# Optimization experiments

Hardware: AMD Instinct MI355X
Metric: run time of the kernel (lower is better)

The kernel has to match this reference:

```python
import jax, jax.numpy as jnp
import numpy as np

T, N, F = 16, 50000, 128
B, S0, S1 = 1024, 10, 5
H0, H1, C = 128, 64, 10
G, DELAYS, K = 8, (1, 3, 5), 5
TAU, ALPHA, VTH = 1.0, 1.0, 1.0


@jax.custom_vjp
def spike_fn(v):
    # Heaviside forward, triangle surrogate backward (alpha=1.0)
    return (v >= VTH).astype(v.dtype)

def _spk_fwd(v):
    return (v >= VTH).astype(v.dtype), v

def _spk_bwd(v, g):
    return (g * ALPHA * jnp.maximum(0.0, 1.0 - jnp.abs(v - VTH)),)

spike_fn.defvjp(_spk_fwd, _spk_bwd)


def setup_inputs() -> dict:
    key = jax.random.key(0)
    ks = jax.random.split(key, 12)
    sc = 0.1
    return {
        'x': jax.random.uniform(ks[0], (T, N, F), jnp.float32),
        'nodes': jax.random.randint(ks[1], (B,), 0, N, jnp.int32),
        'nbr1': jax.random.randint(ks[2], (T, B, S0), 0, N, jnp.int32),
        'nbr2': jax.random.randint(ks[3], (T, B * S0, S1), 0, N, jnp.int32),
        'W_self0': jax.random.normal(ks[4], (F, H0), jnp.float32) * sc,
        'W_neigh0': jax.random.normal(ks[5], (F, H0), jnp.float32) * sc,
        'b0': jnp.zeros((H0,), jnp.float32),
        'W_self1': jax.random.normal(ks[6], (H0, H1), jnp.float32) * sc,
        'W_neigh1': jax.random.normal(ks[7], (H0, H1), jnp.float32) * sc,
        'b1': jnp.zeros((H1,), jnp.float32),
        'delay_logits': jax.random.normal(ks[8], (G, len(DELAYS)), jnp.float32),
        'tsr_dw': jax.random.normal(ks[9], (H1, K), jnp.float32) * sc,
        'tsr_pw': jax.random.normal(ks[10], (H1, C), jnp.float32) * sc,
        'tsr_b': jnp.zeros((C,), jnp.float32),
    }


def reference(x, nodes, nbr1, nbr2, W_self0, W_neigh0, b0, W_self1, W_neigh1, b1,
              delay_logits, tsr_dw, tsr_pw, tsr_b):
    v0_init = jnp.zeros((B + B * S0, H0), x.dtype)
    v1_init = jnp.zeros((B, H1), x.dtype)

    def step(carry, inp):
        v0, v1 = carry
        xt, n1, n2 = inp
        # per-timestep neighbor gathers (irregular access)
        h0 = xt[nodes]                   # [B, F]
        h1 = xt[n1.reshape(-1)]          # [B*S0, F]
        h2 = xt[n2.reshape(-1)]          # [B*S0*S1, F]
        # layer 0: SAGE (mean aggr, concat=False) over both levels, then LIF
        self_x = jnp.concatenate([h0, h1], axis=0)
        neigh = jnp.concatenate([h1.reshape(B, S0, F).mean(1),
                                 h2.reshape(B * S0, S1, F).mean(1)], axis=0)
        a0 = self_x @ W_self0 + neigh @ W_neigh0 + b0
        v0c = v0 + (a0 - v0) / TAU
        spk0 = spike_fn(v0c)
        v0n = v0c * (1.0 - spk0)          # hard reset to 0
        # layer 1: SAGE over level-0 spikes, then LIF
        s_self, s_nb = spk0[:B], spk0[B:]
        a1 = s_self @ W_self1 + s_nb.reshape(B, S0, H0).mean(1) @ W_neigh1 + b1
        v1c = v1 + (a1 - v1) / TAU
        spk1 = spike_fn(v1c)
        v1n = v1c * (1.0 - spk1)
        return (v0n, v1n), spk1

    _, spikes = jax.lax.scan(step, (v0_init, v1_init), (x, nbr1, nbr2))
    spikes = jnp.transpose(spikes, (1, 0, 2))    # [B, T, H1]

    # GroupSparseDelay1D: per-group softmax mixture of time-shifted copies
    w = jax.nn.softmax(delay_logits, axis=-1)     # [G, n_delays]
    wch = jnp.repeat(w, H1 // G, axis=0)          # [H1, n_delays]
    delayed = jnp.zeros_like(spikes)
    for i, d in enumerate(DELAYS):
        shifted = jnp.pad(spikes, ((0, 0), (d, 0), (0, 0)))[:, :T, :]
        delayed = delayed + shifted * wch[:, i]
    spikes = delayed

    # TemporalSeparableReadout: depthwise temporal conv (k=5) + pointwise + mean over T
    xc = jnp.transpose(spikes, (0, 2, 1))         # [B, H1, T]
    y = jax.lax.conv_general_dilated(xc, tsr_dw[:, None, :], (1,), 'SAME',
                                     feature_group_count=H1)  # [B, H1, T]
    out = jnp.einsum('bdt,dc->bc', y, tsr_pw) / T + tsr_b      # [B, C]
    return out
```

## Files before the change

kernel.cpp:

```cpp
#include <hip/hip_runtime.h>
#include <math.h>

#define TT 16
#define NN 50000
#define FF 128
#define BB 1024
#define S0C 10
#define S1C 5
#define H0C 128
#define H1C 64
#define CCC 10
#define R0C (BB + BB*S0C)
#define BANDF 4e-3f

typedef __attribute__((ext_vector_type(8))) short bf16x8;
typedef __attribute__((ext_vector_type(4))) float f32x4;

__device__ __forceinline__ unsigned short bf16_rn(float f) {
  unsigned u = __float_as_uint(f);
  return (unsigned short)((u + 0x7FFFu + ((u >> 16) & 1u)) >> 16);
}
__device__ __forceinline__ void split2(float f, unsigned short& h, unsigned short& l) {
  h = bf16_rn(f);
  float hf = __uint_as_float((unsigned)h << 16);
  l = bf16_rn(f - hf);
}

__global__ __launch_bounds__(256) void k_prep_w(
    const float* __restrict__ Ws0, const float* __restrict__ Wn0,
    unsigned short* __restrict__ Wswz)
{
  const int id = blockIdx.x * 256 + threadIdx.x;
  if (id >= 256 * 128) return;
  const int k = id >> 7, n = id & 127;
  const float wv = (k < 128) ? Ws0[k * H0C + n] : Wn0[(k - 128) * H0C + n];
  unsigned short h, l;
  split2(wv, h, l);
  const int ks = k >> 5, kq = (k >> 3) & 3, j = k & 7;
  const int nt = n >> 4, n16 = n & 15;
  const int idx = (((ks * 8 + nt) * 64) + (kq * 16 + n16)) * 8 + j;
  Wswz[idx] = h;
  Wswz[32768 + idx] = l;
}

__global__ __launch_bounds__(256, 2) void k_layer0(
    const float* __restrict__ x, const int* __restrict__ nodes,
    const int* __restrict__ nbr1, const int* __restrict__ nbr2,
    const unsigned short* __restrict__ Wswz, const float* __restrict__ b0,
    unsigned char* __restrict__ spk0,
    unsigned int* __restrict__ band_list, unsigned int* __restrict__ band_cnt,
    int band_cap)
{
  __shared__ __align__(16) unsigned short Abf[2 * 64 * 256];
  const int t   = blockIdx.y;
  const int r0  = blockIdx.x * 64;
  const int tid = threadIdx.x;
  const float* xt = x + (size_t)t * NN * FF;

  {
    const int rr = tid >> 2, tq = tid & 3, k0 = tq * 32;
    const int r  = r0 + rr;
    const int sw = rr & 7;
    const float* srow;
    float inv;
    int S;
    int ids[10];
    if (r < BB) {
      srow = xt + (size_t)nodes[r] * FF + k0;
      const int* nb = nbr1 + ((size_t)t * BB + r) * S0C;
      #pragma unroll
      for (int s = 0; s < 10; s++) ids[s] = nb[s];
      S = 10; inv = 0.1f;
    } else {
      const int j = r - BB;
      srow = xt + (size_t)nbr1[(size_t)t * BB * S0C + j] * FF + k0;
      const int* nb = nbr2 + ((size_t)t * BB * S0C + j) * S1C;
      #pragma unroll
      for (int s = 0; s < 5; s++) ids[s] = nb[s];
      S = 5; inv = 0.2f;
    }
    float4 a[8];
    #pragma unroll
    for (int q = 0; q < 8; q++) a[q] = make_float4(0.f, 0.f, 0.f, 0.f);
    int s = 0;
    for (; s + 2 <= S; s += 2) {
      const float4* rA = (const float4*)(xt + (size_t)ids[s]     * FF + k0);
      const float4* rB = (const float4*)(xt + (size_t)ids[s + 1] * FF + k0);
      float4 va[8], vb[8];
      #pragma unroll
      for (int q = 0; q < 8; q++) va[q] = rA[q];
      #pragma unroll
      for (int q = 0; q < 8; q++) vb[q] = rB[q];
      #pragma unroll
      for (int q = 0; q < 8; q++) {
        a[q].x += va[q].x + vb[q].x; a[q].y += va[q].y + vb[q].y;
        a[q].z += va[q].z + vb[q].z; a[q].w += va[q].w + vb[q].w;
      }
    }
    if (s < S) {
      const float4* rA = (const float4*)(xt + (size_t)ids[s] * FF + k0);
      #pragma unroll
      for (int q = 0; q < 8; q++) {
        float4 v = rA[q];
        a[q].x += v.x; a[q].y += v.y; a[q].z += v.z; a[q].w += v.w;
      }
    }
    #pragma unroll
    for (int ch = 0; ch < 4; ch++) {
      float v[8] = { a[2*ch].x * inv, a[2*ch].y * inv, a[2*ch].z * inv, a[2*ch].w * inv,
                     a[2*ch+1].x * inv, a[2*ch+1].y * inv, a[2*ch+1].z * inv, a[2*ch+1].w * inv };
      unsigned short h[8], l[8];
      #pragma unroll
      for (int e = 0; e < 8; e++) split2(v[e], h[e], l[e]);
      const int c = 16 + tq * 4 + ch;
      const int idx = rr * 256 + ((c ^ sw) << 3);
      uint4 HW = { (unsigned)h[0] | ((unsigned)h[1] << 16), (unsigned)h[2] | ((unsigned)h[3] << 16),
                   (unsigned)h[4] | ((unsigned)h[5] << 16), (unsigned)h[6] | ((unsigned)h[7] << 16) };
      uint4 LW = { (unsigned)l[0] | ((unsigned)l[1] << 16), (unsigned)l[2] | ((unsigned)l[3] << 16),
                   (unsigned)l[4] | ((unsigned)l[5] << 16), (unsigned)l[6] | ((unsigned)l[7] << 16) };
      *(uint4*)&Abf[idx] = HW;
      *(uint4*)&Abf[16384 + idx] = LW;
    }
    float4 sv[8];
    const float4* sp4 = (const float4*)srow;
    #pragma unroll
    for (int q = 0; q < 8; q++) sv[q] = sp4[q];
    #pragma unroll
    for (int ch = 0; ch < 4; ch++) {
      float v[8] = { sv[2*ch].x, sv[2*ch].y, sv[2*ch].z, sv[2*ch].w,
                     sv[2*ch+1].x, sv[2*ch+1].y, sv[2*ch+1].z, sv[2*ch+1].w };
      unsigned short h[8], l[8];
      #pragma unroll
      for (int e = 0; e < 8; e++) split2(v[e], h[e], l[e]);
      const int c = tq * 4 + ch;
      const int idx = rr * 256 + ((c ^ sw) << 3);
      uint4 HW = { (unsigned)h[0] | ((unsigned)h[1] << 16), (unsigned)h[2] | ((unsigned)h[3] << 16),
                   (unsigned)h[4] | ((unsigned)h[5] << 16), (unsigned)h[6] | ((unsigned)h[7] << 16) };
      uint4 LW = { (unsigned)l[0] | ((unsigned)l[1] << 16), (unsigned)l[2] | ((unsigned)l[3] << 16),
                   (unsigned)l[4] | ((unsigned)l[5] << 16), (unsigned)l[6] | ((unsigned)l[7] << 16) };
      *(uint4*)&Abf[idx] = HW;
      *(uint4*)&Abf[16384 + idx] = LW;
    }
  }
  __syncthreads();

  const int w = tid >> 6, l = tid & 63, m16 = l & 15, quad = l >> 4;
  const int rowl = w * 16 + m16;
  const unsigned short* ArowH = Abf + rowl * 256;
  const unsigned short* ArowL = Abf + 16384 + rowl * 256;
  const int sw = m16 & 7;
  f32x4 acc[8];
  #pragma unroll
  for (int nt = 0; nt < 8; nt++) acc[nt] = (f32x4){0.f, 0.f, 0.f, 0.f};

  for (int ks = 0; ks < 8; ks++) {
    const int c = ks * 4 + quad;
    const int off = (c ^ sw) << 3;
    bf16x8 ah = *(const bf16x8*)(ArowH + off);
    bf16x8 al = *(const bf16x8*)(ArowL + off);
    const unsigned short* wp = Wswz + ((size_t)(ks * 8) * 64 + l) * 8;
    #pragma unroll
    for (int nt = 0; nt < 8; nt++) {
      bf16x8 bh = *(const bf16x8*)(wp + nt * 512);
      bf16x8 bl = *(const bf16x8*)(wp + 32768 + nt * 512);
      acc[nt] = __builtin_amdgcn_mfma_f32_16x16x32_bf16(ah, bh, acc[nt], 0, 0, 0);
      acc[nt] = __builtin_amdgcn_mfma_f32_16x16x32_bf16(al, bh, acc[nt], 0, 0, 0);
      acc[nt] = __builtin_amdgcn_mfma_f32_16x16x32_bf16(ah, bl, acc[nt], 0, 0, 0);
    }
  }

  #pragma unroll
  for (int nt = 0; nt < 8; nt++) {
    const int c = nt * 16 + m16;
    const float bc = b0[c];
    #pragma unroll
    for (int i = 0; i < 4; i++) {
      const int r = r0 + w * 16 + quad * 4 + i;
      const unsigned gr = (unsigned)(t * R0C + r);
      const float av = acc[nt][i] + bc;
      spk0[(size_t)gr * H0C + c] = (unsigned char)(av >= 1.0f);
      if (fabsf(av - 1.0f) < BANDF) {
        unsigned idx = atomicAdd(band_cnt, 1u);
        if ((int)idx < band_cap) band_list[idx] = gr * 128u + (unsigned)c;
      }
    }
  }
}

template<int S>
__device__ __forceinline__ double band_dot(
    const float* xt, int sidx, const int* nb,
    const float* Ws0, const float* Wn0, int c, int lane)
{
  int ids[S];
  #pragma unroll
  for (int s = 0; s < S; s++) ids[s] = nb[s];
  double sum = 0.0;
  #pragma unroll
  for (int h = 0; h < 2; h++) {
    const int k = lane + h * 64;
    const double svv = (double)xt[(size_t)sidx * FF + k];
    double nv = 0.0;
    #pragma unroll
    for (int s = 0; s < S; s++) nv += (double)xt[(size_t)ids[s] * FF + k];
    sum += svv * (double)Ws0[k * H0C + c] + (nv / (double)S) * (double)Wn0[k * H0C + c];
  }
  return sum;
}

__global__ __launch_bounds__(64) void k_recheck(
    const float* __restrict__ x, const int* __restrict__ nodes,
    const int* __restrict__ nbr1, const int* __restrict__ nbr2,
    const float* __restrict__ Ws0, const float* __restrict__ Wn0,
    const float* __restrict__ b0,
    unsigned char* __restrict__ spk0,
    const unsigned int* __restrict__ band_list,
    const unsigned int* __restrict__ band_cnt, int band_cap)
{
  unsigned int n = *band_cnt;
  if (n > (unsigned)band_cap) n = (unsigned)band_cap;
  const int lane = threadIdx.x;
  for (unsigned int i = blockIdx.x; i < n; i += gridDim.x) {
    const unsigned int v = band_list[i];
    const int c = (int)(v & 127u);
    const unsigned int gr = v >> 7;
    const int t = (int)(gr / (unsigned)R0C);
    const int r = (int)(gr - (unsigned)t * (unsigned)R0C);
    const float* xt = x + (size_t)t * NN * FF;
    double sum;
    if (r < BB) {
      sum = band_dot<S0C>(xt, nodes[r], nbr1 + ((size_t)t * BB + r) * S0C,
                          Ws0, Wn0, c, lane);
    } else {
      const int j = r - BB;
      sum = band_dot<S1C>(xt, nbr1[(size_t)t * BB * S0C + j],
                          nbr2 + ((size_t)t * BB * S0C + j) * S1C,
                          Ws0, Wn0, c, lane);
    }
    #pragma unroll
    for (int off = 32; off > 0; off >>= 1) sum += __shfl_down(sum, off);
    if (lane == 0) {
      const double a = sum + (double)b0[c];
      spk0[(size_t)gr * H0C + c] = (a >= 1.0) ? (unsigned char)1 : (unsigned char)0;
    }
  }
}

__global__ __launch_bounds__(256, 2) void k_layer1(
    const unsigned char* __restrict__ spk0,
    const float* __restrict__ Ws1, const float* __restrict__ Wn1,
    const float* __restrict__ b1, float* __restrict__ spk1)
{
  __shared__ float  WsL[H0C * H1C];
  __shared__ float  WnL[H0C * H1C];
  __shared__ float  ssf[4][H0C];
  __shared__ double md[4][H0C];
  const int tid   = threadIdx.x;
  const int t     = blockIdx.y;
  const int bbase = blockIdx.x * 16;
  for (int i = tid; i < H0C * H1C; i += 256) { WsL[i] = Ws1[i]; WnL[i] = Wn1[i]; }
  __syncthreads();
  const int wave = tid >> 6, lane = tid & 63;
  for (int it = 0; it < 4; it++) {
    const int b = bbase + it * 4 + wave;
    #pragma unroll
    for (int h = 0; h < 2; h++) {
      const int k = lane + h * 64;
      ssf[wave][k] = (float)spk0[((size_t)t * R0C + b) * H0C + k];
      int cnt = 0;
      #pragma unroll
      for (int s = 0; s < S0C; s++)
        cnt += spk0[((size_t)t * R0C + BB + b * S0C + s) * H0C + k];
      md[wave][k] = (double)cnt / 10.0;
    }
    __syncthreads();
    double aS0 = 0.0, aS1 = 0.0, aN0 = 0.0, aN1 = 0.0;
    #pragma unroll 4
    for (int k = 0; k < H0C; k += 2) {
      aS0 += (double)ssf[wave][k]     * (double)WsL[k * H1C + lane];
      aS1 += (double)ssf[wave][k + 1] * (double)WsL[(k + 1) * H1C + lane];
      aN0 += md[wave][k]     * (double)WnL[k * H1C + lane];
      aN1 += md[wave][k + 1] * (double)WnL[(k + 1) * H1C + lane];
    }
    const double acc = (double)b1[lane] + ((aS0 + aS1) + (aN0 + aN1));
    spk1[((size_t)b * TT + t) * H1C + lane] = (acc >= 1.0) ? 1.0f : 0.0f;
    __syncthreads();
  }
}

__global__ __launch_bounds__(64) void k_readout(
    const float* __restrict__ spk1, const float* __restrict__ logits,
    const float* __restrict__ dw, const float* __restrict__ pw,
    const float* __restrict__ tb, float* __restrict__ out)
{
  __shared__ double ysL[H1C];
  const int b = blockIdx.x, d = threadIdx.x;
  const float* lg = logits + (d >> 3) * 3;
  const double l0 = (double)lg[0], l1 = (double)lg[1], l2 = (double)lg[2];
  const double mx = fmax(l0, fmax(l1, l2));
  const double e0 = exp(l0 - mx), e1 = exp(l1 - mx), e2 = exp(l2 - mx);
  const double se = e0 + e1 + e2;
  const double w0 = e0 / se, w1 = e1 / se, w2 = e2 / se;

  float sp[TT];
  #pragma unroll
  for (int t = 0; t < TT; t++) sp[t] = spk1[((size_t)b * TT + t) * H1C + d];

  double dl[TT];
  #pragma unroll
  for (int t = 0; t < TT; t++) {
    double v = 0.0;
    if (t >= 1) v += (double)sp[t - 1] * w0;
    if (t >= 3) v += (double)sp[t - 3] * w1;
    if (t >= 5) v += (double)sp[t - 5] * w2;
    dl[t] = v;
  }
  double kw[5];
  #pragma unroll
  for (int k = 0; k < 5; k++) kw[k] = (double)dw[d * 5 + k];
  double ys = 0.0;
  #pragma unroll
  for (int t = 0; t < TT; t++) {
    double y = 0.0;
    #pragma unroll
    for (int k = 0; k < 5; k++) {
      const int t2 = t + k - 2;
      if (t2 >= 0 && t2 < TT) y += dl[t2] * kw[k];
    }
    ys += y;
  }
  ysL[d] = ys;
  __syncthreads();
  if (d < CCC) {
    double acc = 0.0;
    for (int dd = 0; dd < H1C; dd++) acc += ysL[dd] * (double)pw[dd * CCC + d];
    out[(size_t)b * CCC + d] = (float)(acc / (double)TT + (double)tb[d]);
  }
}

extern "C" void kernel_launch(void* const* d_in, const int* in_sizes, int n_in,
                              void* d_out, int out_size, void* d_ws, size_t ws_size,
                              hipStream_t stream)
{
  const float* x      = (const float*)d_in[0];
  const int*   nodes  = (const int*)d_in[1];
  const int*   nbr1   = (const int*)d_in[2];
  const int*   nbr2   = (const int*)d_in[3];
  const float* Ws0    = (const float*)d_in[4];
  const float* Wn0    = (const float*)d_in[5];
  const float* b0     = (const float*)d_in[6];
  const float* Ws1    = (const float*)d_in[7];
  const float* Wn1    = (const float*)d_in[8];
  const float* b1     = (const float*)d_in[9];
  const float* logits = (const float*)d_in[10];
  const float* dw     = (const float*)d_in[11];
  const float* pw     = (const float*)d_in[12];
  const float* tb     = (const float*)d_in[13];
  float* out = (float*)d_out;

  char* ws = (char*)d_ws;
  unsigned char*  spk0      = (unsigned char*)ws;
  float*          spk1      = (float*)(ws + 23068672);
  unsigned short* Wswz      = (unsigned short*)(ws + 27262976);
  unsigned int*   band_cnt  = (unsigned int*)(ws + 27394048);
  unsigned int*   band_list = (unsigned int*)(ws + 27394304);
  const long long rem = (long long)ws_size - 27394304LL;
  const int band_cap = rem > 0 ? (int)((rem / 4 < (long long)(1 << 20)) ? rem / 4 : (long long)(1 << 20)) : 0;

  hipMemsetAsync(band_cnt, 0, 4, stream);
  k_prep_w <<<dim3(128),      256, 0, stream>>>(Ws0, Wn0, Wswz);
  k_layer0 <<<dim3(176, 16),  256, 0, stream>>>(x, nodes, nbr1, nbr2, Wswz, b0,
                                                spk0, band_list, band_cnt, band_cap);
  k_recheck<<<dim3(2048),     64,  0, stream>>>(x, nodes, nbr1, nbr2, Ws0, Wn0, b0,
                                                spk0, band_list, band_cnt, band_cap);
  k_layer1 <<<dim3(64, 16),   256, 0, stream>>>(spk0, Ws1, Wn1, b1, spk1);
  k_readout<<<dim3(1024),     64,  0, stream>>>(spk1, logits, dw, pw, tb, out);
}
```

Baseline: 995.0 us.

## Split layer0 into half-K passes, transpose recheck weights, coarsen layer1 blocks

Layer 0 now stages the self and neighbor halves of the A operand one at a time in a half-size LDS buffer and runs MFMA on each half in turn. This halves LDS use and raises the launch bound to 3 blocks per SM to improve occupancy. The recheck kernel reads transposed fp32 weights so lanes access contiguous memory, and the weight-prep kernel zeroes the band counter in place of a separate memset. Layer 1 processes 64 nodes per block so each block loads the weights once for more nodes, and it drops the barriers between per-wave iterations. The narrower recheck band cuts recheck work but risks missing near-threshold values that bf16x3 rounding could flip.

```diff
diff --git a/kernel.cpp b/kernel.cpp
--- a/kernel.cpp
+++ b/kernel.cpp
@@ -11,7 +11,7 @@
 #define H1C 64
 #define CCC 10
 #define R0C (BB + BB*S0C)
-#define BANDF 4e-3f
+#define BANDF 2e-3f
 
 typedef __attribute__((ext_vector_type(8))) short bf16x8;
 typedef __attribute__((ext_vector_type(4))) float f32x4;
@@ -28,12 +28,17 @@
 
 __global__ __launch_bounds__(256) void k_prep_w(
     const float* __restrict__ Ws0, const float* __restrict__ Wn0,
-    unsigned short* __restrict__ Wswz)
+    unsigned short* __restrict__ Wswz,
+    float* __restrict__ WsT, float* __restrict__ WnT,
+    unsigned int* __restrict__ band_cnt)
 {
   const int id = blockIdx.x * 256 + threadIdx.x;
+  if (id == 0) *band_cnt = 0u;
   if (id >= 256 * 128) return;
   const int k = id >> 7, n = id & 127;
   const float wv = (k < 128) ? Ws0[k * H0C + n] : Wn0[(k - 128) * H0C + n];
+  if (k < 128) WsT[n * 128 + k] = wv;
+  else         WnT[n * 128 + (k - 128)] = wv;
   unsigned short h, l;
   split2(wv, h, l);
   const int ks = k >> 5, kq = (k >> 3) & 3, j = k & 7;
@@ -43,7 +48,80 @@
   Wswz[32768 + idx] = l;
 }
 
-__global__ __launch_bounds__(256, 2) void k_layer0(
+__device__ __forceinline__ void split_write4(
+    unsigned short* __restrict__ Abf, int rr, int tq,
+    const float4 a[8], float inv)
+{
+  const int sw = rr & 7;
+  #pragma unroll
+  for (int ch = 0; ch < 4; ch++) {
+    float v[8] = { a[2*ch].x * inv, a[2*ch].y * inv, a[2*ch].z * inv, a[2*ch].w * inv,
+                   a[2*ch+1].x * inv, a[2*ch+1].y * inv, a[2*ch+1].z * inv, a[2*ch+1].w * inv };
+    unsigned short h[8], l[8];
+    #pragma unroll
+    for (int e = 0; e < 8; e++) split2(v[e], h[e], l[e]);
+    const int c = tq * 4 + ch;
+    const int idx = rr * 128 + ((c ^ sw) << 3);
+    uint4 HW = { (unsigned)h[0] | ((unsigned)h[1] << 16), (unsigned)h[2] | ((unsigned)h[3] << 16),
+                 (unsigned)h[4] | ((unsigned)h[5] << 16), (unsigned)h[6] | ((unsigned)h[7] << 16) };
+    uint4 LW = { (unsigned)l[0] | ((unsigned)l[1] << 16), (unsigned)l[2] | ((unsigned)l[3] << 16),
+                 (unsigned)l[4] | ((unsigned)l[5] << 16), (unsigned)l[6] | ((unsigned)l[7] << 16) };
+    *(uint4*)&Abf[idx] = HW;
+    *(uint4*)&Abf[8192 + idx] = LW;
+  }
+}
+
+template<int S>
+__device__ __forceinline__ void gather_neigh_half(
+    const float* __restrict__ xt, const int* __restrict__ nb, float inv,
+    unsigned short* __restrict__ Abf, int rr, int tq)
+{
+  const int k0 = tq * 32;
+  int ids[S];
+  #pragma unroll
+  for (int s = 0; s < S; s++) ids[s] = nb[s];
+  float4 a[8];
+  #pragma unroll
+  for (int q = 0; q < 8; q++) a[q] = make_float4(0.f, 0.f, 0.f, 0.f);
+  #pragma unroll
+  for (int s = 0; s < S; s++) {
+    const float4* rA = (const float4*)(xt + (size_t)ids[s] * FF + k0);
+    float4 v[8];
+    #pragma unroll
+    for (int q = 0; q < 8; q++) v[q] = rA[q];
+    #pragma unroll
+    for (int q = 0; q < 8; q++) {
+      a[q].x += v[q].x; a[q].y += v[q].y; a[q].z += v[q].z; a[q].w += v[q].w;
+    }
+  }
+  split_write4(Abf, rr, tq, a, inv);
+}
+
+__device__ __forceinline__ void mfma_half(
+    const unsigned short* __restrict__ ArowH,
+    const unsigned short* __restrict__ ArowL,
+    const unsigned short* __restrict__ Wswz,
+    int half, int l, int quad, int swm, f32x4 acc[8])
+{
+  #pragma unroll
+  for (int ksl = 0; ksl < 4; ksl++) {
+    const int c = ksl * 4 + quad;
+    const int off = (c ^ swm) << 3;
+    bf16x8 ah = *(const bf16x8*)(ArowH + off);
+    bf16x8 al = *(const bf16x8*)(ArowL + off);
+    const unsigned short* wp = Wswz + ((size_t)((half * 4 + ksl) * 8) * 64 + l) * 8;
+    #pragma unroll
+    for (int nt = 0; nt < 8; nt++) {
+      bf16x8 bh = *(const bf16x8*)(wp + nt * 512);
+      bf16x8 bl = *(const bf16x8*)(wp + 32768 + nt * 512);
+      acc[nt] = __builtin_amdgcn_mfma_f32_16x16x32_bf16(ah, bh, acc[nt], 0, 0, 0);
+      acc[nt] = __builtin_amdgcn_mfma_f32_16x16x32_bf16(al, bh, acc[nt], 0, 0, 0);
+      acc[nt] = __builtin_amdgcn_mfma_f32_16x16x32_bf16(ah, bl, acc[nt], 0, 0, 0);
+    }
+  }
+}
+
+__global__ __launch_bounds__(256, 3) void k_layer0(
     const float* __restrict__ x, const int* __restrict__ nodes,
     const int* __restrict__ nbr1, const int* __restrict__ nbr2,
     const unsigned short* __restrict__ Wswz, const float* __restrict__ b0,
@@ -51,123 +129,43 @@
     unsigned int* __restrict__ band_list, unsigned int* __restrict__ band_cnt,
     int band_cap)
 {
-  __shared__ __align__(16) unsigned short Abf[2 * 64 * 256];
+  __shared__ __align__(16) unsigned short Abf[2 * 64 * 128];
   const int t   = blockIdx.y;
   const int r0  = blockIdx.x * 64;
   const int tid = threadIdx.x;
   const float* xt = x + (size_t)t * NN * FF;
-
-  {
-    const int rr = tid >> 2, tq = tid & 3, k0 = tq * 32;
-    const int r  = r0 + rr;
-    const int sw = rr & 7;
-    const float* srow;
-    float inv;
-    int S;
-    int ids[10];
-    if (r < BB) {
-      srow = xt + (size_t)nodes[r] * FF + k0;
-      const int* nb = nbr1 + ((size_t)t * BB + r) * S0C;
-      #pragma unroll
-      for (int s = 0; s < 10; s++) ids[s] = nb[s];
-      S = 10; inv = 0.1f;
-    } else {
-      const int j = r - BB;
-      srow = xt + (size_t)nbr1[(size_t)t * BB * S0C + j] * FF + k0;
-      const int* nb = nbr2 + ((size_t)t * BB * S0C + j) * S1C;
-      #pragma unroll
-      for (int s = 0; s < 5; s++) ids[s] = nb[s];
-      S = 5; inv = 0.2f;
-    }
-    float4 a[8];
-    #pragma unroll
-    for (int q = 0; q < 8; q++) a[q] = make_float4(0.f, 0.f, 0.f, 0.f);
-    int s = 0;
-    for (; s + 2 <= S; s += 2) {
-      const float4* rA = (const float4*)(xt + (size_t)ids[s]     * FF + k0);
-      const float4* rB = (const float4*)(xt + (size_t)ids[s + 1] * FF + k0);
-      float4 va[8], vb[8];
-      #pragma unroll
-      for (int q = 0; q < 8; q++) va[q] = rA[q];
-      #pragma unroll
-      for (int q = 0; q < 8; q++) vb[q] = rB[q];
-      #pragma unroll
-      for (int q = 0; q < 8; q++) {
-        a[q].x += va[q].x + vb[q].x; a[q].y += va[q].y + vb[q].y;
-        a[q].z += va[q].z + vb[q].z; a[q].w += va[q].w + vb[q].w;
-      }
-    }
-    if (s < S) {
-      const float4* rA = (const float4*)(xt + (size_t)ids[s] * FF + k0);
-      #pragma unroll
-      for (int q = 0; q < 8; q++) {
-        float4 v = rA[q];
-        a[q].x += v.x; a[q].y += v.y; a[q].z += v.z; a[q].w += v.w;
-      }
-    }
-    #pragma unroll
-    for (int ch = 0; ch < 4; ch++) {
-      float v[8] = { a[2*ch].x * inv, a[2*ch].y * inv, a[2*ch].z * inv, a[2*ch].w * inv,
-                     a[2*ch+1].x * inv, a[2*ch+1].y * inv, a[2*ch+1].z * inv, a[2*ch+1].w * inv };
-      unsigned short h[8], l[8];
-      #pragma unroll
-      for (int e = 0; e < 8; e++) split2(v[e], h[e], l[e]);
-      const int c = 16 + tq * 4 + ch;
-      const int idx = rr * 256 + ((c ^ sw) << 3);
-      uint4 HW = { (unsigned)h[0] | ((unsigned)h[1] << 16), (unsigned)h[2] | ((unsigned)h[3] << 16),
-                   (unsigned)h[4] | ((unsigned)h[5] << 16), (unsigned)h[6] | ((unsigned)h[7] << 16) };
-      uint4 LW = { (unsigned)l[0] | ((unsigned)l[1] << 16), (unsigned)l[2] | ((unsigned)l[3] << 16),
-                   (unsigned)l[4] | ((unsigned)l[5] << 16), (unsigned)l[6] | ((unsigned)l[7] << 16) };
-      *(uint4*)&Abf[idx] = HW;
-      *(uint4*)&Abf[16384 + idx] = LW;
-    }
-    float4 sv[8];
-    const float4* sp4 = (const float4*)srow;
-    #pragma unroll
-    for (int q = 0; q < 8; q++) sv[q] = sp4[q];
-    #pragma unroll
-    for (int ch = 0; ch < 4; ch++) {
-      float v[8] = { sv[2*ch].x, sv[2*ch].y, sv[2*ch].z, sv[2*ch].w,
-                     sv[2*ch+1].x, sv[2*ch+1].y, sv[2*ch+1].z, sv[2*ch+1].w };
-      unsigned short h[8], l[8];
-      #pragma unroll
-      for (int e = 0; e < 8; e++) split2(v[e], h[e], l[e]);
-      const int c = tq * 4 + ch;
-      const int idx = rr * 256 + ((c ^ sw) << 3);
-      uint4 HW = { (unsigned)h[0] | ((unsigned)h[1] << 16), (unsigned)h[2] | ((unsigned)h[3] << 16),
-                   (unsigned)h[4] | ((unsigned)h[5] << 16), (unsigned)h[6] | ((unsigned)h[7] << 16) };
-      uint4 LW = { (unsigned)l[0] | ((unsigned)l[1] << 16), (unsigned)l[2] | ((unsigned)l[3] << 16),
-                   (unsigned)l[4] | ((unsigned)l[5] << 16), (unsigned)l[6] | ((unsigned)l[7] << 16) };
-      *(uint4*)&Abf[idx] = HW;
-      *(uint4*)&Abf[16384 + idx] = LW;
-    }
-  }
-  __syncthreads();
+  const int rr = tid >> 2, tq = tid & 3, k0 = tq * 32;
+  const int r  = r0 + rr;
 
   const int w = tid >> 6, l = tid & 63, m16 = l & 15, quad = l >> 4;
   const int rowl = w * 16 + m16;
-  const unsigned short* ArowH = Abf + rowl * 256;
-  const unsigned short* ArowL = Abf + 16384 + rowl * 256;
-  const int sw = m16 & 7;
+  const unsigned short* ArowH = Abf + rowl * 128;
+  const unsigned short* ArowL = Abf + 8192 + rowl * 128;
+  const int swm = m16 & 7;
   f32x4 acc[8];
   #pragma unroll
   for (int nt = 0; nt < 8; nt++) acc[nt] = (f32x4){0.f, 0.f, 0.f, 0.f};
 
-  for (int ks = 0; ks < 8; ks++) {
-    const int c = ks * 4 + quad;
-    const int off = (c ^ sw) << 3;
-    bf16x8 ah = *(const bf16x8*)(ArowH + off);
-    bf16x8 al = *(const bf16x8*)(ArowL + off);
-    const unsigned short* wp = Wswz + ((size_t)(ks * 8) * 64 + l) * 8;
-    #pragma unroll
-    for (int nt = 0; nt < 8; nt++) {
-      bf16x8 bh = *(const bf16x8*)(wp + nt * 512);
-      bf16x8 bl = *(const bf16x8*)(wp + 32768 + nt * 512);
-      acc[nt] = __builtin_amdgcn_mfma_f32_16x16x32_bf16(ah, bh, acc[nt], 0, 0, 0);
-      acc[nt] = __builtin_amdgcn_mfma_f32_16x16x32_bf16(al, bh, acc[nt], 0, 0, 0);
-      acc[nt] = __builtin_amdgcn_mfma_f32_16x16x32_bf16(ah, bl, acc[nt], 0, 0, 0);
-    }
-  }
+  {
+    const float* srow;
+    if (r < BB) srow = xt + (size_t)nodes[r] * FF + k0;
+    else        srow = xt + (size_t)nbr1[(size_t)t * BB * S0C + (r - BB)] * FF + k0;
+    const float4* sp4 = (const float4*)srow;
+    float4 sv[8];
+    #pragma unroll
+    for (int q = 0; q < 8; q++) sv[q] = sp4[q];
+    split_write4(Abf, rr, tq, sv, 1.0f);
+  }
+  __syncthreads();
+  mfma_half(ArowH, ArowL, Wswz, 0, l, quad, swm, acc);
+  __syncthreads();
+
+  if (r < BB)
+    gather_neigh_half<S0C>(xt, nbr1 + ((size_t)t * BB + r) * S0C, 0.1f, Abf, rr, tq);
+  else
+    gather_neigh_half<S1C>(xt, nbr2 + ((size_t)t * BB * S0C + (r - BB)) * S1C, 0.2f, Abf, rr, tq);
+  __syncthreads();
+  mfma_half(ArowH, ArowL, Wswz, 1, l, quad, swm, acc);
 
   #pragma unroll
   for (int nt = 0; nt < 8; nt++) {
@@ -175,8 +173,8 @@
     const float bc = b0[c];
     #pragma unroll
     for (int i = 0; i < 4; i++) {
-      const int r = r0 + w * 16 + quad * 4 + i;
-      const unsigned gr = (unsigned)(t * R0C + r);
+      const int rr2 = r0 + w * 16 + quad * 4 + i;
+      const unsigned gr = (unsigned)(t * R0C + rr2);
       const float av = acc[nt][i] + bc;
       spk0[(size_t)gr * H0C + c] = (unsigned char)(av >= 1.0f);
       if (fabsf(av - 1.0f) < BANDF) {
@@ -190,7 +188,7 @@
 template<int S>
 __device__ __forceinline__ double band_dot(
     const float* xt, int sidx, const int* nb,
-    const float* Ws0, const float* Wn0, int c, int lane)
+    const float* WsT, const float* WnT, int c, int lane)
 {
   int ids[S];
   #pragma unroll
@@ -203,7 +201,7 @@
     double nv = 0.0;
     #pragma unroll
     for (int s = 0; s < S; s++) nv += (double)xt[(size_t)ids[s] * FF + k];
-    sum += svv * (double)Ws0[k * H0C + c] + (nv / (double)S) * (double)Wn0[k * H0C + c];
+    sum += svv * (double)WsT[c * 128 + k] + (nv / (double)S) * (double)WnT[c * 128 + k];
   }
   return sum;
 }
@@ -211,7 +209,7 @@
 __global__ __launch_bounds__(64) void k_recheck(
     const float* __restrict__ x, const int* __restrict__ nodes,
     const int* __restrict__ nbr1, const int* __restrict__ nbr2,
-    const float* __restrict__ Ws0, const float* __restrict__ Wn0,
+    const float* __restrict__ WsT, const float* __restrict__ WnT,
     const float* __restrict__ b0,
     unsigned char* __restrict__ spk0,
     const unsigned int* __restrict__ band_list,
@@ -230,12 +228,12 @@
     double sum;
     if (r < BB) {
       sum = band_dot<S0C>(xt, nodes[r], nbr1 + ((size_t)t * BB + r) * S0C,
-                          Ws0, Wn0, c, lane);
+                          WsT, WnT, c, lane);
     } else {
       const int j = r - BB;
       sum = band_dot<S1C>(xt, nbr1[(size_t)t * BB * S0C + j],
                           nbr2 + ((size_t)t * BB * S0C + j) * S1C,
-                          Ws0, Wn0, c, lane);
+                          WsT, WnT, c, lane);
     }
     #pragma unroll
     for (int off = 32; off > 0; off >>= 1) sum += __shfl_down(sum, off);
@@ -257,11 +255,17 @@
   __shared__ double md[4][H0C];
   const int tid   = threadIdx.x;
   const int t     = blockIdx.y;
-  const int bbase = blockIdx.x * 16;
-  for (int i = tid; i < H0C * H1C; i += 256) { WsL[i] = Ws1[i]; WnL[i] = Wn1[i]; }
+  const int bbase = blockIdx.x * 64;
+  {
+    const float4* s4 = (const float4*)Ws1;
+    const float4* n4 = (const float4*)Wn1;
+    float4* sL = (float4*)WsL;
+    float4* nL = (float4*)WnL;
+    for (int i = tid; i < H0C * H1C / 4; i += 256) { sL[i] = s4[i]; nL[i] = n4[i]; }
+  }
   __syncthreads();
   const int wave = tid >> 6, lane = tid & 63;
-  for (int it = 0; it < 4; it++) {
+  for (int it = 0; it < 16; it++) {
     const int b = bbase + it * 4 + wave;
     #pragma unroll
     for (int h = 0; h < 2; h++) {
@@ -273,7 +277,6 @@
         cnt += spk0[((size_t)t * R0C + BB + b * S0C + s) * H0C + k];
       md[wave][k] = (double)cnt / 10.0;
     }
-    __syncthreads();
     double aS0 = 0.0, aS1 = 0.0, aN0 = 0.0, aN1 = 0.0;
     #pragma unroll 4
     for (int k = 0; k < H0C; k += 2) {
@@ -284,7 +287,6 @@
     }
     const double acc = (double)b1[lane] + ((aS0 + aS1) + (aN0 + aN1));
     spk1[((size_t)b * TT + t) * H1C + lane] = (acc >= 1.0) ? 1.0f : 0.0f;
-    __syncthreads();
   }
 }
 
@@ -362,17 +364,18 @@
   unsigned char*  spk0      = (unsigned char*)ws;
   float*          spk1      = (float*)(ws + 23068672);
   unsigned short* Wswz      = (unsigned short*)(ws + 27262976);
-  unsigned int*   band_cnt  = (unsigned int*)(ws + 27394048);
-  unsigned int*   band_list = (unsigned int*)(ws + 27394304);
-  const long long rem = (long long)ws_size - 27394304LL;
+  float*          WsT       = (float*)(ws + 27394048);
+  float*          WnT       = (float*)(ws + 27459584);
+  unsigned int*   band_cnt  = (unsigned int*)(ws + 27525120);
+  unsigned int*   band_list = (unsigned int*)(ws + 27525376);
+  const long long rem = (long long)ws_size - 27525376LL;
   const int band_cap = rem > 0 ? (int)((rem / 4 < (long long)(1 << 20)) ? rem / 4 : (long long)(1 << 20)) : 0;
 
-  hipMemsetAsync(band_cnt, 0, 4, stream);
-  k_prep_w <<<dim3(128),      256, 0, stream>>>(Ws0, Wn0, Wswz);
+  k_prep_w <<<dim3(128),      256, 0, stream>>>(Ws0, Wn0, Wswz, WsT, WnT, band_cnt);
   k_layer0 <<<dim3(176, 16),  256, 0, stream>>>(x, nodes, nbr1, nbr2, Wswz, b0,
                                                 spk0, band_list, band_cnt, band_cap);
-  k_recheck<<<dim3(2048),     64,  0, stream>>>(x, nodes, nbr1, nbr2, Ws0, Wn0, b0,
+  k_recheck<<<dim3(2048),     64,  0, stream>>>(x, nodes, nbr1, nbr2, WsT, WnT, b0,
                                                 spk0, band_list, band_cnt, band_cap);
-  k_layer1 <<<dim3(64, 16),   256, 0, stream>>>(spk0, Ws1, Wn1, b1, spk1);
+  k_layer1 <<<dim3(16, 16),   256, 0, stream>>>(spk0, Ws1, Wn1, b1, spk1);
   k_readout<<<dim3(1024),     64,  0, stream>>>(spk1, logits, dw, pw, tb, out);
 }
```

New measurement: 820.1 us. 1.21x faster.
